# Kernel optimization log

Measured on AMD Instinct MI355X. Metric: run time of the kernel, lower is better.

The kernel has to match this reference:

```python
import jax, jax.numpy as jnp
import numpy as np

B, L, HID, NH = 4, 1024, 768, 12
HD = HID // NH  # head dim 64
VOCAB, MPE = 30, 2048
NW, WL = 8, 16
BETA = 1.0


def setup_inputs() -> dict:
    key = jax.random.key(0)
    ks = jax.random.split(key, 10)
    hidden_states = jax.random.normal(ks[0], (B, L, HID), dtype=jnp.float32)
    attention_mask = jnp.zeros((B, 1, 1, L), dtype=jnp.float32)
    distance = jax.random.randint(ks[1], (B, L, L), 0, 1022, dtype=jnp.int32)
    random_walk = jax.random.randint(ks[2], (B, L, NW, WL), 0, VOCAB, dtype=jnp.int32)
    anonymous_random_walk = jax.random.randint(ks[3], (B, L, NW, WL), 0, VOCAB, dtype=jnp.int32)
    s = 0.02
    Wq = jax.random.normal(ks[4], (HID, HID), dtype=jnp.float32) * s
    Wk = jax.random.normal(ks[5], (HID, HID), dtype=jnp.float32) * s
    Wv = jax.random.normal(ks[6], (HID, HID), dtype=jnp.float32) * s
    bq = jnp.zeros((HID,), jnp.float32)
    bk = jnp.zeros((HID,), jnp.float32)
    bv = jnp.zeros((HID,), jnp.float32)
    node_emb = jax.random.normal(ks[7], (VOCAB, HID), dtype=jnp.float32) * s
    node_emb = node_emb.at[0].set(0.0)  # padding_idx=0
    dist_emb = jax.random.normal(ks[8], (MPE, NH), dtype=jnp.float32) * s
    dist_emb = dist_emb.at[0].set(0.0)  # padding_idx=0
    return dict(hidden_states=hidden_states, attention_mask=attention_mask,
                Wq=Wq, bq=bq, Wk=Wk, bk=bk, Wv=Wv, bv=bv,
                node_emb=node_emb, dist_emb=dist_emb,
                distance=distance, random_walk=random_walk,
                anonymous_random_walk=anonymous_random_walk)


def _heads(x):  # [B,L,HID] -> [B,NH,L,HD]
    return x.reshape(B, L, NH, HD).transpose(0, 2, 1, 3)


def _walk_bias(walk, node_emb):
    # walk: [B,L,NW,WL] int -> embed [B,L,NW,WL,HID] -> sum dims (2,3) -> [B,L,HID]
    pe = jnp.sum(node_emb[walk], axis=(2, 3))
    e = _heads(pe)  # [B,NH,L,HD]
    return jnp.einsum('bhid,bhjd->bhij', e, e)


def reference(hidden_states, attention_mask, Wq, bq, Wk, bk, Wv, bv,
              node_emb, dist_emb, distance, random_walk, anonymous_random_walk):
    q = _heads(hidden_states @ Wq.T + bq)
    k = _heads(hidden_states @ Wk.T + bk)
    v = _heads(hidden_states @ Wv.T + bv)
    scores = jnp.einsum('bhid,bhjd->bhij', q, k) / np.sqrt(HD).astype(np.float32)
    # distance RPE: [B,L,L,NH] -> [B,NH,L,L]
    bias = dist_emb[distance + 1].transpose(0, 3, 1, 2)
    bias = bias + _walk_bias(random_walk, node_emb)
    bias = bias + _walk_bias(anonymous_random_walk, node_emb)
    scores = scores + bias * BETA + attention_mask
    probs = jax.nn.softmax(scores, axis=-1)
    ctx = jnp.einsum('bhij,bhjd->bhid', probs, v)
    return ctx.transpose(0, 2, 1, 3).reshape(B, L, HID)
```

## Files before the change

### kernel.cpp

```cpp
#include <hip/hip_runtime.h>
#include <hip/hip_bf16.h>

#define LL 1024
#define HID 768
#define NH 12
#define HD 64
#define KAUG 192
#define NBH 48

typedef unsigned int u32;
typedef unsigned short u16;
typedef __bf16 bf16_t;
typedef bf16_t bf16x8 __attribute__((ext_vector_type(8)));
typedef float f32x4 __attribute__((ext_vector_type(4)));
typedef u32 u32x4 __attribute__((ext_vector_type(4)));

__device__ __forceinline__ u16 f2b(float f) {
    union { float f; u32 u; } v; v.f = f;
    u32 r = v.u + 0x7fffu + ((v.u >> 16) & 1u);
    return (u16)(r >> 16);
}
__device__ __forceinline__ bf16x8 load8s(const u16* p) {
    return __builtin_bit_cast(bf16x8, *reinterpret_cast<const u32x4*>(p));
}
__device__ __forceinline__ void cvt4_store_v(u16* dst, float4 f) {
    ushort4 o;
    o.x = f2b(f.x); o.y = f2b(f.y); o.z = f2b(f.z); o.w = f2b(f.w);
    *reinterpret_cast<ushort4*>(dst) = o;
}

__global__ __launch_bounds__(256) void k_qkv(const float* __restrict__ hs,
                                             const float* __restrict__ Wq, const float* __restrict__ Wk,
                                             const float* __restrict__ Wv,
                                             const float* __restrict__ bq, const float* __restrict__ bk,
                                             const float* __restrict__ bv,
                                             u16* __restrict__ Qa, u16* __restrict__ Ka,
                                             u16* __restrict__ Vt) {
    __shared__ __align__(16) u16 smem[18432];
    u16* a_s = smem;
    u16* b_s = smem + 9216;
    int m0 = blockIdx.x * 128;
    int nt = blockIdx.y;
    int which = nt / 6;
    int n0w = (nt % 6) * 128;
    const float* W    = (which == 0) ? Wq : (which == 1) ? Wk : Wv;
    const float* bias = (which == 0) ? bq : (which == 1) ? bk : bv;
    int tid = threadIdx.x;
    int wave = tid >> 6, lane = tid & 63, l15 = lane & 15, qd = lane >> 4;
    int wm = wave >> 1, wn = wave & 1;

    int srow = tid >> 4, scol = (tid & 15) * 4;

    f32x4 acc[4][4];
    for (int i = 0; i < 4; i++)
        for (int j = 0; j < 4; j++) acc[i][j] = f32x4{0.f, 0.f, 0.f, 0.f};

    float4 pa[8], pb[8];
#pragma unroll
    for (int it = 0; it < 8; it++) {
        int row = srow + it * 16;
        pa[it] = *reinterpret_cast<const float4*>(&hs[(size_t)(m0 + row) * 768 + scol]);
        pb[it] = *reinterpret_cast<const float4*>(&W[(size_t)(n0w + row) * 768 + scol]);
    }
    for (int k0 = 0; k0 < 768; k0 += 64) {
        __syncthreads();
#pragma unroll
        for (int it = 0; it < 8; it++) {
            int row = srow + it * 16;
            cvt4_store_v(&a_s[row * 72 + scol], pa[it]);
            cvt4_store_v(&b_s[row * 72 + scol], pb[it]);
        }
        __syncthreads();
        if (k0 < 704) {
            int k1 = k0 + 64;
#pragma unroll
            for (int it = 0; it < 8; it++) {
                int row = srow + it * 16;
                pa[it] = *reinterpret_cast<const float4*>(&hs[(size_t)(m0 + row) * 768 + k1 + scol]);
                pb[it] = *reinterpret_cast<const float4*>(&W[(size_t)(n0w + row) * 768 + k1 + scol]);
            }
        }
        for (int kk = 0; kk < 2; kk++) {
            bf16x8 af[4], bf[4];
            for (int i = 0; i < 4; i++) af[i] = load8s(&a_s[(wm * 64 + i * 16 + l15) * 72 + kk * 32 + qd * 8]);
            for (int j = 0; j < 4; j++) bf[j] = load8s(&b_s[(wn * 64 + j * 16 + l15) * 72 + kk * 32 + qd * 8]);
            for (int i = 0; i < 4; i++)
                for (int j = 0; j < 4; j++)
                    acc[i][j] = __builtin_amdgcn_mfma_f32_16x16x32_bf16(af[i], bf[j], acc[i][j], 0, 0, 0);
        }
    }
    __syncthreads();
    int b = m0 >> 10, l0b = m0 & 1023;
    if (which != 2) {
        float qscale = (which == 0) ? 0.125f : 1.0f;
        for (int i = 0; i < 4; i++) {
            int m_loc = wm * 64 + i * 16 + qd * 4;
            for (int j = 0; j < 4; j++) {
                int n_loc = wn * 64 + j * 16 + l15;
                float bv_ = bias[n0w + n_loc];
                for (int r = 0; r < 4; r++)
                    smem[(m_loc + r) * 136 + n_loc] = f2b((acc[i][j][r] + bv_) * qscale);
            }
        }
        __syncthreads();
        u16* dstbuf = (which == 0) ? Qa : Ka;
        for (int it = 0; it < 8; it++) {
            int c = tid + it * 256;
            int row = c >> 4, col = (c & 15) * 8;
            u32x4 w = *reinterpret_cast<u32x4*>(&smem[row * 136 + col]);
            int nn = n0w + col;
            int h = nn >> 6, d = nn & 63;
            size_t dst = ((size_t)(b * NH + h) * LL + (l0b + row)) * KAUG + d;
            *reinterpret_cast<u32x4*>(&dstbuf[dst]) = w;
        }
    } else {
        for (int i = 0; i < 4; i++) {
            int m_loc = wm * 64 + i * 16 + qd * 4;
            for (int j = 0; j < 4; j++) {
                int n_loc = wn * 64 + j * 16 + l15;
                float bv_ = bias[n0w + n_loc];
                for (int r = 0; r < 4; r++)
                    smem[n_loc * 136 + (m_loc + r)] = f2b(acc[i][j][r] + bv_);
            }
        }
        __syncthreads();
        for (int it = 0; it < 8; it++) {
            int c = tid + it * 256;
            int n = c >> 4, m_off = (c & 15) * 8;
            u32x4 w = *reinterpret_cast<u32x4*>(&smem[n * 136 + m_off]);
            int nn = n0w + n;
            int h = nn >> 6, d = nn & 63;
            size_t dst = ((size_t)(b * NH + h) * HD + d) * LL + (l0b + m_off);
            *reinterpret_cast<u32x4*>(&Vt[dst]) = w;
        }
    }
}

__global__ __launch_bounds__(256) void k_pe(const int* __restrict__ rw,
                                            const int* __restrict__ arw,
                                            const float* __restrict__ node_emb,
                                            u16* __restrict__ Qa, u16* __restrict__ Ka) {
    int m = blockIdx.x;
    __shared__ int hist[64];
    __shared__ float c1[32], c2[32];
    int t = threadIdx.x;
    if (t < 64) hist[t] = 0;
    __syncthreads();
    if (t < 128) atomicAdd(&hist[rw[m * 128 + t] & 31], 1);
    else         atomicAdd(&hist[32 + (arw[m * 128 + (t - 128)] & 31)], 1);
    __syncthreads();
    if (t < 64) {
        if (t < 32) c1[t] = (float)hist[t];
        else        c2[t - 32] = (float)hist[t];
    }
    __syncthreads();
    int b = m >> 10, l = m & 1023;
    for (int c = t; c < 768; c += 256) {
        float s1 = 0.f, s2 = 0.f;
        for (int v = 0; v < 30; v++) {
            float ne = node_emb[v * 768 + c];
            s1 += c1[v] * ne;
            s2 += c2[v] * ne;
        }
        int h = c >> 6, d = c & 63;
        size_t base = ((size_t)(b * NH + h) * LL + l) * KAUG;
        u16 e1 = f2b(s1), e2 = f2b(s2);
        Qa[base + 64 + d] = e1;  Ka[base + 64 + d] = e1;
        Qa[base + 128 + d] = e2; Ka[base + 128 + d] = e2;
    }
}

__global__ __launch_bounds__(256) void k_attn(const u16* __restrict__ Qa, const u16* __restrict__ Ka,
                                              const u16* __restrict__ Vt,
                                              const int* __restrict__ distance,
                                              const float* __restrict__ dist_emb,
                                              const float* __restrict__ mask,
                                              void* __restrict__ outv, int f32mode) {
    __shared__ __align__(16) u16 ka_s[64][200];
    __shared__ __align__(16) u16 vt_s[64][72];
    __shared__ __align__(16) u16 p_s[4][16][72];
    __shared__ float distcol[2048];

    int itile = blockIdx.x;
    int bh = blockIdx.y;
    int b = bh / NH, h = bh % NH;
    int tid = threadIdx.x, wave = tid >> 6, lane = tid & 63, l15 = lane & 15, qd = lane >> 4;

    const u16* Qh = Qa + (size_t)bh * LL * KAUG;
    const u16* Kh = Ka + (size_t)bh * LL * KAUG;
    const u16* Vh = Vt + (size_t)bh * HD * LL;
    const int* distb = distance + (size_t)b * LL * LL;
    const float* maskb = mask + (size_t)b * LL;

    for (int t = tid; t < 2048; t += 256) distcol[t] = dist_emb[t * NH + h];

    int krow = (tid * 6 + 0) / 24;
    (void)krow;

    int i0 = itile * 64 + wave * 16;
    bf16x8 aq[6];
    for (int ks = 0; ks < 6; ks++)
        aq[ks] = load8s(&Qh[(size_t)(i0 + l15) * KAUG + ks * 32 + qd * 8]);

    f32x4 o[4];
    for (int i = 0; i < 4; i++) o[i] = f32x4{0.f, 0.f, 0.f, 0.f};
    float m_i[4], l_i[4];
    for (int r = 0; r < 4; r++) { m_i[r] = -1e30f; l_i[r] = 0.f; }

    u32x4 kbuf[6], vbuf[2];
#pragma unroll
    for (int it = 0; it < 6; it++) {
        int c = tid + it * 256;
        int row = c / 24, col = (c % 24) * 8;
        kbuf[it] = *reinterpret_cast<const u32x4*>(&Kh[(size_t)row * KAUG + col]);
    }
#pragma unroll
    for (int it = 0; it < 2; it++) {
        int c = tid + it * 256;
        int d = c >> 3, col = (c & 7) * 8;
        vbuf[it] = *reinterpret_cast<const u32x4*>(&Vh[(size_t)d * LL + col]);
    }
    int dpre[16]; float mpre[4];
    for (int nf = 0; nf < 4; nf++) {
        int j_abs = nf * 16 + l15;
        mpre[nf] = maskb[j_abs];
        for (int r = 0; r < 4; r++)
            dpre[nf * 4 + r] = distb[(size_t)(i0 + qd * 4 + r) * LL + j_abs];
    }

    for (int jt = 0; jt < 16; jt++) {
        int j0 = jt * 64;
        __syncthreads();
#pragma unroll
        for (int it = 0; it < 6; it++) {
            int c = tid + it * 256;
            int row = c / 24, col = (c % 24) * 8;
            *reinterpret_cast<u32x4*>(&ka_s[row][col]) = kbuf[it];
        }
#pragma unroll
        for (int it = 0; it < 2; it++) {
            int c = tid + it * 256;
            int d = c >> 3, col = (c & 7) * 8;
            *reinterpret_cast<u32x4*>(&vt_s[d][col]) = vbuf[it];
        }
        __syncthreads();
        int dcur[16]; float mcur[4];
        for (int u_ = 0; u_ < 16; u_++) dcur[u_] = dpre[u_];
        for (int u_ = 0; u_ < 4; u_++)  mcur[u_] = mpre[u_];
        if (jt < 15) {
            int j0n = j0 + 64;
#pragma unroll
            for (int it = 0; it < 6; it++) {
                int c = tid + it * 256;
                int row = c / 24, col = (c % 24) * 8;
                kbuf[it] = *reinterpret_cast<const u32x4*>(&Kh[(size_t)(j0n + row) * KAUG + col]);
            }
#pragma unroll
            for (int it = 0; it < 2; it++) {
                int c = tid + it * 256;
                int d = c >> 3, col = (c & 7) * 8;
                vbuf[it] = *reinterpret_cast<const u32x4*>(&Vh[(size_t)d * LL + j0n + col]);
            }
            for (int nf = 0; nf < 4; nf++) {
                int j_abs = j0n + nf * 16 + l15;
                mpre[nf] = maskb[j_abs];
                for (int r = 0; r < 4; r++)
                    dpre[nf * 4 + r] = distb[(size_t)(i0 + qd * 4 + r) * LL + j_abs];
            }
        }

        f32x4 s[4];
        for (int nf = 0; nf < 4; nf++) {
            f32x4 accv = f32x4{0.f, 0.f, 0.f, 0.f};
            for (int ks = 0; ks < 6; ks++) {
                bf16x8 bfrag = load8s(&ka_s[nf * 16 + l15][ks * 32 + qd * 8]);
                accv = __builtin_amdgcn_mfma_f32_16x16x32_bf16(aq[ks], bfrag, accv, 0, 0, 0);
            }
            s[nf] = accv;
        }
        for (int nf = 0; nf < 4; nf++)
            for (int r = 0; r < 4; r++)
                s[nf][r] += distcol[dcur[nf * 4 + r] + 1] + mcur[nf];
        float mx[4];
        for (int r = 0; r < 4; r++) {
            float v = fmaxf(fmaxf(s[0][r], s[1][r]), fmaxf(s[2][r], s[3][r]));
            for (int off = 1; off < 16; off <<= 1) v = fmaxf(v, __shfl_xor(v, off));
            mx[r] = v;
        }
        float alpha[4], rs[4];
        for (int r = 0; r < 4; r++) {
            float mnew = fmaxf(m_i[r], mx[r]);
            alpha[r] = __expf(m_i[r] - mnew);
            m_i[r] = mnew;
            rs[r] = 0.f;
        }
        for (int nf = 0; nf < 4; nf++)
            for (int r = 0; r < 4; r++) {
                float p = __expf(s[nf][r] - m_i[r]);
                rs[r] += p;
                p_s[wave][qd * 4 + r][nf * 16 + l15] = f2b(p);
            }
        for (int r = 0; r < 4; r++) {
            float v = rs[r];
            for (int off = 1; off < 16; off <<= 1) v += __shfl_xor(v, off);
            l_i[r] = l_i[r] * alpha[r] + v;
        }
        for (int df = 0; df < 4; df++)
            for (int r = 0; r < 4; r++) o[df][r] *= alpha[r];
        __builtin_amdgcn_sched_barrier(0);
        asm volatile("" ::: "memory");
        for (int kstep = 0; kstep < 2; kstep++) {
            bf16x8 ap = load8s(&p_s[wave][l15][kstep * 32 + qd * 8]);
            for (int df = 0; df < 4; df++) {
                bf16x8 bv_ = load8s(&vt_s[df * 16 + l15][kstep * 32 + qd * 8]);
                o[df] = __builtin_amdgcn_mfma_f32_16x16x32_bf16(ap, bv_, o[df], 0, 0, 0);
            }
        }
    }
    for (int df = 0; df < 4; df++) {
        int d = df * 16 + l15;
        for (int r = 0; r < 4; r++) {
            int i_abs = i0 + qd * 4 + r;
            float v = o[df][r] / l_i[r];
            size_t idx = ((size_t)(b * LL) + i_abs) * HID + h * 64 + d;
            if (f32mode) ((float*)outv)[idx] = v;
            else         ((u16*)outv)[idx] = f2b(v);
        }
    }
}

extern "C" void kernel_launch(void* const* d_in, const int* in_sizes, int n_in,
                              void* d_out, int out_size, void* d_ws, size_t ws_size,
                              hipStream_t stream) {
    const float* hs       = (const float*)d_in[0];
    const float* mask     = (const float*)d_in[1];
    const float* Wq       = (const float*)d_in[2];
    const float* bq       = (const float*)d_in[3];
    const float* Wk       = (const float*)d_in[4];
    const float* bk       = (const float*)d_in[5];
    const float* Wv       = (const float*)d_in[6];
    const float* bv       = (const float*)d_in[7];
    const float* node_emb = (const float*)d_in[8];
    const float* dist_emb = (const float*)d_in[9];
    const int* distance   = (const int*)d_in[10];
    const int* rw         = (const int*)d_in[11];
    const int* arw        = (const int*)d_in[12];

    int f32mode = 0;
    {
        hipDeviceptr_t base = nullptr; size_t sz = 0;
        if (hipMemGetAddressRange(&base, &sz, (hipDeviceptr_t)d_out) == hipSuccess) {
            size_t off = (size_t)((char*)d_out - (char*)base);
            if (sz - off >= (size_t)out_size * 4u) f32mode = 1;
        }
    }

    u16* Qa = (u16*)d_ws;
    u16* Ka = Qa + (size_t)NBH * LL * KAUG;
    u16* Vt = Ka + (size_t)NBH * LL * KAUG;

    k_qkv<<<dim3(32, 18), dim3(256), 0, stream>>>(hs, Wq, Wk, Wv, bq, bk, bv, Qa, Ka, Vt);
    k_pe<<<dim3(4096), dim3(256), 0, stream>>>(rw, arw, node_emb, Qa, Ka);
    k_attn<<<dim3(16, 48), dim3(256), 0, stream>>>(Qa, Ka, Vt, distance, dist_emb, mask, d_out, f32mode);
}
```

Baseline: 250.1 us.

## Pre-convert GEMM inputs to bf16 and gather distance bias from global memory

Adds a conversion kernel that turns hidden states and the QKV weights into bf16 in workspace, so the projection GEMM loads half the bytes and skips in-loop conversion. The attention kernel drops its shared-memory per-head distance-embedding table and instead gathers the bias values directly from the global dist_emb array each tile. This frees shared memory and the per-block table fill, at the cost of an extra launch, extra workspace traffic and latency-exposed scattered global loads.

```diff
diff --git a/kernel.cpp b/kernel.cpp
--- a/kernel.cpp
+++ b/kernel.cpp
@@ -29,9 +29,25 @@
     *reinterpret_cast<ushort4*>(dst) = o;
 }
 
-__global__ __launch_bounds__(256) void k_qkv(const float* __restrict__ hs,
-                                             const float* __restrict__ Wq, const float* __restrict__ Wk,
+__global__ __launch_bounds__(256) void k_cvt(const float* __restrict__ hs,
+                                             const float* __restrict__ Wq,
+                                             const float* __restrict__ Wk,
                                              const float* __restrict__ Wv,
+                                             u16* __restrict__ hs_b, u16* __restrict__ Wq_b,
+                                             u16* __restrict__ Wk_b, u16* __restrict__ Wv_b) {
+    int seg = blockIdx.y;
+    const float* src = (seg == 0) ? hs : (seg == 1) ? Wq : (seg == 2) ? Wk : Wv;
+    u16* dst         = (seg == 0) ? hs_b : (seg == 1) ? Wq_b : (seg == 2) ? Wk_b : Wv_b;
+    int nchunk = (seg == 0) ? 786432 : 147456;
+    int c = blockIdx.x * 256 + threadIdx.x;
+    if (c >= nchunk) return;
+    float4 f = *reinterpret_cast<const float4*>(&src[(size_t)c * 4]);
+    cvt4_store_v(&dst[(size_t)c * 4], f);
+}
+
+__global__ __launch_bounds__(256) void k_qkv(const u16* __restrict__ hs_b,
+                                             const u16* __restrict__ Wq_b, const u16* __restrict__ Wk_b,
+                                             const u16* __restrict__ Wv_b,
                                              const float* __restrict__ bq, const float* __restrict__ bk,
                                              const float* __restrict__ bv,
                                              u16* __restrict__ Qa, u16* __restrict__ Ka,
@@ -43,41 +59,42 @@
     int nt = blockIdx.y;
     int which = nt / 6;
     int n0w = (nt % 6) * 128;
-    const float* W    = (which == 0) ? Wq : (which == 1) ? Wk : Wv;
+    const u16* W      = (which == 0) ? Wq_b : (which == 1) ? Wk_b : Wv_b;
     const float* bias = (which == 0) ? bq : (which == 1) ? bk : bv;
     int tid = threadIdx.x;
     int wave = tid >> 6, lane = tid & 63, l15 = lane & 15, qd = lane >> 4;
     int wm = wave >> 1, wn = wave & 1;
 
-    int srow = tid >> 4, scol = (tid & 15) * 4;
-
     f32x4 acc[4][4];
     for (int i = 0; i < 4; i++)
         for (int j = 0; j < 4; j++) acc[i][j] = f32x4{0.f, 0.f, 0.f, 0.f};
 
-    float4 pa[8], pb[8];
-#pragma unroll
-    for (int it = 0; it < 8; it++) {
-        int row = srow + it * 16;
-        pa[it] = *reinterpret_cast<const float4*>(&hs[(size_t)(m0 + row) * 768 + scol]);
-        pb[it] = *reinterpret_cast<const float4*>(&W[(size_t)(n0w + row) * 768 + scol]);
+    u32x4 pa[4], pb[4];
+#pragma unroll
+    for (int it = 0; it < 4; it++) {
+        int c = tid + it * 256;
+        int row = c >> 3, col = (c & 7) * 8;
+        pa[it] = *reinterpret_cast<const u32x4*>(&hs_b[(size_t)(m0 + row) * 768 + col]);
+        pb[it] = *reinterpret_cast<const u32x4*>(&W[(size_t)(n0w + row) * 768 + col]);
     }
     for (int k0 = 0; k0 < 768; k0 += 64) {
         __syncthreads();
 #pragma unroll
-        for (int it = 0; it < 8; it++) {
-            int row = srow + it * 16;
-            cvt4_store_v(&a_s[row * 72 + scol], pa[it]);
-            cvt4_store_v(&b_s[row * 72 + scol], pb[it]);
+        for (int it = 0; it < 4; it++) {
+            int c = tid + it * 256;
+            int row = c >> 3, col = (c & 7) * 8;
+            *reinterpret_cast<u32x4*>(&a_s[row * 72 + col]) = pa[it];
+            *reinterpret_cast<u32x4*>(&b_s[row * 72 + col]) = pb[it];
         }
         __syncthreads();
         if (k0 < 704) {
             int k1 = k0 + 64;
 #pragma unroll
-            for (int it = 0; it < 8; it++) {
-                int row = srow + it * 16;
-                pa[it] = *reinterpret_cast<const float4*>(&hs[(size_t)(m0 + row) * 768 + k1 + scol]);
-                pb[it] = *reinterpret_cast<const float4*>(&W[(size_t)(n0w + row) * 768 + k1 + scol]);
+            for (int it = 0; it < 4; it++) {
+                int c = tid + it * 256;
+                int row = c >> 3, col = (c & 7) * 8;
+                pa[it] = *reinterpret_cast<const u32x4*>(&hs_b[(size_t)(m0 + row) * 768 + k1 + col]);
+                pb[it] = *reinterpret_cast<const u32x4*>(&W[(size_t)(n0w + row) * 768 + k1 + col]);
             }
         }
         for (int kk = 0; kk < 2; kk++) {
@@ -179,7 +196,6 @@
     __shared__ __align__(16) u16 ka_s[64][200];
     __shared__ __align__(16) u16 vt_s[64][72];
     __shared__ __align__(16) u16 p_s[4][16][72];
-    __shared__ float distcol[2048];
 
     int itile = blockIdx.x;
     int bh = blockIdx.y;
@@ -191,11 +207,7 @@
     const u16* Vh = Vt + (size_t)bh * HD * LL;
     const int* distb = distance + (size_t)b * LL * LL;
     const float* maskb = mask + (size_t)b * LL;
-
-    for (int t = tid; t < 2048; t += 256) distcol[t] = dist_emb[t * NH + h];
-
-    int krow = (tid * 6 + 0) / 24;
-    (void)krow;
+    const float* debh = dist_emb + h;
 
     int i0 = itile * 64 + wave * 16;
     bf16x8 aq[6];
@@ -247,6 +259,10 @@
         int dcur[16]; float mcur[4];
         for (int u_ = 0; u_ < 16; u_++) dcur[u_] = dpre[u_];
         for (int u_ = 0; u_ < 4; u_++)  mcur[u_] = mpre[u_];
+        float bias_cur[16];
+#pragma unroll
+        for (int u_ = 0; u_ < 16; u_++)
+            bias_cur[u_] = debh[(size_t)(dcur[u_] + 1) * NH];
         if (jt < 15) {
             int j0n = j0 + 64;
 #pragma unroll
@@ -280,7 +296,7 @@
         }
         for (int nf = 0; nf < 4; nf++)
             for (int r = 0; r < 4; r++)
-                s[nf][r] += distcol[dcur[nf * 4 + r] + 1] + mcur[nf];
+                s[nf][r] += bias_cur[nf * 4 + r] + mcur[nf];
         float mx[4];
         for (int r = 0; r < 4; r++) {
             float v = fmaxf(fmaxf(s[0][r], s[1][r]), fmaxf(s[2][r], s[3][r]));
@@ -355,11 +371,16 @@
         }
     }
 
-    u16* Qa = (u16*)d_ws;
-    u16* Ka = Qa + (size_t)NBH * LL * KAUG;
-    u16* Vt = Ka + (size_t)NBH * LL * KAUG;
-
-    k_qkv<<<dim3(32, 18), dim3(256), 0, stream>>>(hs, Wq, Wk, Wv, bq, bk, bv, Qa, Ka, Vt);
+    u16* Qa   = (u16*)d_ws;
+    u16* Ka   = Qa + (size_t)NBH * LL * KAUG;
+    u16* Vt   = Ka + (size_t)NBH * LL * KAUG;
+    u16* hs_b = Vt + (size_t)NBH * HD * LL;
+    u16* Wq_b = hs_b + (size_t)4096 * 768;
+    u16* Wk_b = Wq_b + (size_t)768 * 768;
+    u16* Wv_b = Wk_b + (size_t)768 * 768;
+
+    k_cvt<<<dim3(3072, 4), dim3(256), 0, stream>>>(hs, Wq, Wk, Wv, hs_b, Wq_b, Wk_b, Wv_b);
+    k_qkv<<<dim3(32, 18), dim3(256), 0, stream>>>(hs_b, Wq_b, Wk_b, Wv_b, bq, bk, bv, Qa, Ka, Vt);
     k_pe<<<dim3(4096), dim3(256), 0, stream>>>(rw, arw, node_emb, Qa, Ka);
     k_attn<<<dim3(16, 48), dim3(256), 0, stream>>>(Qa, Ka, Vt, distance, dist_emb, mask, d_out, f32mode);
 }
```

Result: slower. 266.5 us (+6.5%).
